# Kernel optimization log

Measured on AMD Instinct MI355X. Metric: run time of the kernel, lower is better.

The kernel has to match this reference:

```python
import jax, jax.numpy as jnp
import numpy as np
import math

B, S, D = 1, 4096, 2048
H, KVH, HD = 32, 8, 64
W = 512            # sliding window size (== block size)
THETA = 10000.0
EPS = 1e-5
INTER = 5632
PRE_SCALE = 1.0 / math.sqrt(2.0)


def setup_inputs() -> dict:
    key = jax.random.key(0)
    ks = jax.random.split(key, 8)
    def w(k, shape, fan_in):
        return jax.random.normal(k, shape, jnp.float32) * (fan_in ** -0.5)
    return {
        "hidden_states": jax.random.normal(ks[0], (B, S, D), jnp.float32),
        "mixer_norm_w": jnp.ones((D,), jnp.float32),
        "wq": w(ks[1], (D, H * HD), D),
        "wk": w(ks[2], (D, KVH * HD), D),
        "wv": w(ks[3], (D, KVH * HD), D),
        "wo": w(ks[4], (H * HD, D), H * HD),
        "mlp_norm_w": jnp.ones((D,), jnp.float32),
        "w_gate": w(ks[5], (D, 2 * INTER), D),
        "w_down": w(ks[6], (INTER, D), INTER),
    }


def rmsnorm(x, w, eps=EPS):
    return x * jax.lax.rsqrt(jnp.mean(x * x, axis=-1, keepdims=True) + eps) * w


def rope(x):
    # x: [B, S, h, HD]; rotate-half RoPE
    half = HD // 2
    inv_freq = 1.0 / (THETA ** (jnp.arange(0, HD, 2, dtype=jnp.float32) / HD))
    freqs = jnp.arange(S, dtype=jnp.float32)[:, None] * inv_freq[None, :]  # [S, half]
    cos = jnp.cos(freqs)[None, :, None, :]
    sin = jnp.sin(freqs)[None, :, None, :]
    x1, x2 = x[..., :half], x[..., half:]
    return jnp.concatenate([x1 * cos - x2 * sin, x2 * cos + x1 * sin], axis=-1)


def sliding_attention(x, wq, wk, wv, wo):
    # x already pre-scaled; returns attn output (pre /pre_scale)
    q = (x @ wq).reshape(B, S, H, HD)
    k = (x @ wk).reshape(B, S, KVH, HD)
    v = (x @ wv).reshape(B, S, KVH, HD)
    q, k = rope(q), rope(k)
    rep = H // KVH
    k = jnp.repeat(k, rep, axis=2)  # [B,S,H,HD]
    v = jnp.repeat(v, rep, axis=2)
    nb = S // W
    qb = q.reshape(B, nb, W, H, HD)
    kb = k.reshape(B, nb, W, H, HD)
    vb = v.reshape(B, nb, W, H, HD)
    zeros = jnp.zeros((B, 1, W, H, HD), q.dtype)
    kw = jnp.concatenate([jnp.concatenate([zeros, kb[:, :-1]], axis=1), kb], axis=2)  # [B,nb,2W,H,HD]
    vw = jnp.concatenate([jnp.concatenate([zeros, vb[:, :-1]], axis=1), vb], axis=2)
    # local mask [nb, W, 2W]
    blk = jnp.arange(nb)[:, None, None]
    q_pos = blk * W + jnp.arange(W)[None, :, None]
    k_pos = blk * W - W + jnp.arange(2 * W)[None, None, :]
    mask = (k_pos >= 0) & (k_pos <= q_pos) & (q_pos - k_pos < W)
    scores = jnp.einsum("bnqhd,bnkhd->bhnqk", qb, kw) * (HD ** -0.5)
    scores = jnp.where(mask[None, None], scores, jnp.finfo(scores.dtype).min)
    p = jax.nn.softmax(scores, axis=-1)
    out = jnp.einsum("bhnqk,bnkhd->bnqhd", p, vw).reshape(B, S, H * HD)
    return out @ wo


def reference(hidden_states, mixer_norm_w, wq, wk, wv, wo, mlp_norm_w, w_gate, w_down):
    residual = hidden_states
    x = rmsnorm(hidden_states, mixer_norm_w)
    attn_out = sliding_attention(x * PRE_SCALE, wq, wk, wv, wo) / PRE_SCALE
    h = residual + attn_out
    xn = rmsnorm(h, mlp_norm_w)
    gv = xn @ w_gate
    gate, y = gv[..., :INTER], gv[..., INTER:]
    mlp_out = (jax.nn.silu(gate) * y) @ w_down
    return h + mlp_out
```

## Files before the change

### kernel.cpp

```cpp
#include <hip/hip_runtime.h>
#include <stdint.h>

typedef __attribute__((ext_vector_type(8))) short s16x8;
typedef __attribute__((ext_vector_type(4))) float f32x4;

#define GLD_LDS16(gp, lp) __builtin_amdgcn_global_load_lds( \
    (__attribute__((address_space(1))) void*)(void*)(gp), \
    (__attribute__((address_space(3))) void*)(lp), 16, 0, 0)

__device__ __forceinline__ float b2f(unsigned short s) {
    unsigned int u = ((unsigned int)s) << 16;
    return __builtin_bit_cast(float, u);
}
__device__ __forceinline__ unsigned short f2b(float f) {
    unsigned int u = __builtin_bit_cast(unsigned int, f);
    u = (u + 0x7FFFu + ((u >> 16) & 1u)) >> 16;
    return (unsigned short)u;
}
__device__ __forceinline__ f32x4 mfma16(s16x8 a, s16x8 b, f32x4 c) {
    return __builtin_amdgcn_mfma_f32_16x16x32_bf16(a, b, c, 0, 0, 0);
}
template <int N> __device__ __forceinline__ void waitvm() {
    if constexpr (N == 2) asm volatile("s_waitcnt vmcnt(2)" ::: "memory");
    else if constexpr (N == 3) asm volatile("s_waitcnt vmcnt(3)" ::: "memory");
    else if constexpr (N == 4) asm volatile("s_waitcnt vmcnt(4)" ::: "memory");
}

__global__ __launch_bounds__(256) void rmsnorm_bf16(
    const float* __restrict__ x, const float* __restrict__ wgt,
    unsigned short* __restrict__ out)
{
    const int row = blockIdx.x;
    const int t = threadIdx.x;
    const float* xr = x + (size_t)row * 2048;
    float4 a = *(const float4*)(xr + t * 8);
    float4 b = *(const float4*)(xr + t * 8 + 4);
    float ss = a.x*a.x + a.y*a.y + a.z*a.z + a.w*a.w
             + b.x*b.x + b.y*b.y + b.z*b.z + b.w*b.w;
    #pragma unroll
    for (int d = 1; d < 64; d <<= 1) ss += __shfl_xor(ss, d);
    __shared__ float red[4];
    if ((t & 63) == 0) red[t >> 6] = ss;
    __syncthreads();
    float tot = red[0] + red[1] + red[2] + red[3];
    float inv = rsqrtf(tot * (1.0f / 2048.0f) + 1e-5f);
    float vals[8] = {a.x, a.y, a.z, a.w, b.x, b.y, b.z, b.w};
    const float* wr_ = wgt + t * 8;
    s16x8 ov;
    #pragma unroll
    for (int j = 0; j < 8; ++j) ov[j] = (short)f2b(vals[j] * inv * wr_[j]);
    *(s16x8*)(out + (size_t)row * 2048 + t * 8) = ov;
}

__global__ __launch_bounds__(256) void transpose_to_bf16(
    const float* __restrict__ in, unsigned short* __restrict__ out, int K, int N)
{
    __shared__ float tile[32][33];
    int n0 = blockIdx.x * 32, k0 = blockIdx.y * 32;
    int r = threadIdx.x >> 5, c = threadIdx.x & 31;
    #pragma unroll
    for (int i = 0; i < 4; ++i)
        tile[r + i * 8][c] = in[(size_t)(k0 + r + i * 8) * N + n0 + c];
    __syncthreads();
    #pragma unroll
    for (int i = 0; i < 4; ++i)
        out[(size_t)(n0 + r + i * 8) * K + k0 + c] = f2b(tile[c][r + i * 8]);
}

template <int BN, int EPI>
__global__ __launch_bounds__(512, 2) void gemmq(
    const unsigned short* __restrict__ A,
    const unsigned short* __restrict__ B,
    void* __restrict__ Cv,
    const float* __restrict__ ADD,
    int N, int K)
{
    constexpr int WN  = BN / 4;
    constexpr int HN  = WN / 2;
    constexpr int NJQ = WN / 32;
    constexpr int LBH = NJQ;
    constexpr int NBU = BN / 64;
    constexpr int ABUF = 256 * 64;
    constexpr int BBUF = BN * 64;
    __shared__ __align__(16) unsigned short As[2 * ABUF];
    __shared__ __align__(16) unsigned short Bs[2 * BBUF];

    const int t = threadIdx.x;
    const int l = t & 63, w = t >> 6;
    const int l15 = l & 15, lg = l >> 4;
    const int wr = w >> 2, wc = w & 3;
    const int x7 = l15 & 7;
    const int cc0 = ((lg) ^ x7) << 3;
    const int cc1 = ((4 | lg) ^ x7) << 3;

    const int nwg = (int)gridDim.x;
    const int orig = (int)blockIdx.x;
    const int q8 = nwg >> 3, r8 = nwg & 7;
    const int xcd = orig & 7, lid = orig >> 3;
    const int wg = (xcd < r8 ? xcd * (q8 + 1) : r8 * (q8 + 1) + (xcd - r8) * q8) + lid;
    const int m0 = (wg & 15) * 256;
    const int n0 = (wg >> 4) * BN;

    const int tr = t >> 3;
    const int scol = ((t & 7) ^ (tr & 7)) << 3;
    const unsigned short* pA[4];
    #pragma unroll
    for (int u = 0; u < 4; ++u) {
        const int lrow = u * 64 + tr;
        const int g = ((lrow >> 6) & 1) * 128 + (lrow >> 7) * 64 + (lrow & 63);
        pA[u] = A + (size_t)(m0 + g) * K + scol;
    }
    const unsigned short* pB[NBU];
    #pragma unroll
    for (int u = 0; u < NBU; ++u) {
        const int lrow = u * 64 + tr;
        const int h = lrow / (BN / 2), rem = lrow % (BN / 2);
        const int g = (rem / HN) * WN + h * HN + (rem % HN);
        pB[u] = B + (size_t)(n0 + g) * K + scol;
    }

    f32x4 acc[2][2][4][NJQ] = {};
    s16x8 aF[4][2];
    s16x8 bF[2][NJQ][2];

    const int NT = K / 64;

    GLD_LDS16(pA[0], &As[0 * 4096 + t * 8]);
    GLD_LDS16(pA[1], &As[1 * 4096 + t * 8]);
    #pragma unroll
    for (int u = 0; u < NBU / 2; ++u) GLD_LDS16(pB[u], &Bs[u * 4096 + t * 8]);
    GLD_LDS16(pA[2], &As[2 * 4096 + t * 8]);
    GLD_LDS16(pA[3], &As[3 * 4096 + t * 8]);
    #pragma unroll
    for (int u = NBU / 2; u < NBU; ++u) GLD_LDS16(pB[u], &Bs[u * 4096 + t * 8]);
    waitvm<2 + LBH>();
    __builtin_amdgcn_s_barrier();

    for (int kt = 0; kt < NT; ++kt) {
        const int rb  = (kt & 1) ? ABUF : 0;
        const int rbB = (kt & 1) ? BBUF : 0;
        const int wb  = ABUF - rb;
        const int wbB = BBUF - rbB;
        const int knext = (kt + 1 < NT ? kt + 1 : kt) * 64;

        #pragma unroll
        for (int i = 0; i < 4; ++i) {
            const int lr = wr * 64 + i * 16 + l15;
            aF[i][0] = *(const s16x8*)&As[rb + lr * 64 + cc0];
            aF[i][1] = *(const s16x8*)&As[rb + lr * 64 + cc1];
        }
        #pragma unroll
        for (int j = 0; j < NJQ; ++j) {
            const int lr = wc * HN + j * 16 + l15;
            bF[0][j][0] = *(const s16x8*)&Bs[rbB + lr * 64 + cc0];
            bF[0][j][1] = *(const s16x8*)&Bs[rbB + lr * 64 + cc1];
        }
        GLD_LDS16(pA[0] + knext, &As[wb + 0 * 4096 + t * 8]);
        GLD_LDS16(pA[1] + knext, &As[wb + 1 * 4096 + t * 8]);
        if constexpr (NJQ == 2) asm volatile("s_waitcnt lgkmcnt(8)" ::: "memory");
        __builtin_amdgcn_s_barrier();
        asm volatile("s_waitcnt lgkmcnt(0)" ::: "memory");
        __builtin_amdgcn_sched_barrier(0);
        __builtin_amdgcn_s_setprio(1);
        #pragma unroll
        for (int kk = 0; kk < 2; ++kk)
            #pragma unroll
            for (int i = 0; i < 4; ++i)
                #pragma unroll
                for (int j = 0; j < NJQ; ++j)
                    acc[0][0][i][j] = mfma16(aF[i][kk], bF[0][j][kk], acc[0][0][i][j]);
        __builtin_amdgcn_s_setprio(0);
        __builtin_amdgcn_sched_barrier(0);
        waitvm<2>();
        __builtin_amdgcn_s_barrier();

        #pragma unroll
        for (int j = 0; j < NJQ; ++j) {
            const int lr = (BN / 2) + wc * HN + j * 16 + l15;
            bF[1][j][0] = *(const s16x8*)&Bs[rbB + lr * 64 + cc0];
            bF[1][j][1] = *(const s16x8*)&Bs[rbB + lr * 64 + cc1];
        }
        #pragma unroll
        for (int u = 0; u < NBU / 2; ++u)
            GLD_LDS16(pB[u] + knext, &Bs[wbB + u * 4096 + t * 8]);
        __builtin_amdgcn_s_barrier();
        asm volatile("s_waitcnt lgkmcnt(0)" ::: "memory");
        __builtin_amdgcn_sched_barrier(0);
        __builtin_amdgcn_s_setprio(1);
        #pragma unroll
        for (int kk = 0; kk < 2; ++kk)
            #pragma unroll
            for (int i = 0; i < 4; ++i)
                #pragma unroll
                for (int j = 0; j < NJQ; ++j)
                    acc[0][1][i][j] = mfma16(aF[i][kk], bF[1][j][kk], acc[0][1][i][j]);
        __builtin_amdgcn_s_setprio(0);
        __builtin_amdgcn_sched_barrier(0);
        __builtin_amdgcn_s_barrier();

        #pragma unroll
        for (int i = 0; i < 4; ++i) {
            const int lr = 128 + wr * 64 + i * 16 + l15;
            aF[i][0] = *(const s16x8*)&As[rb + lr * 64 + cc0];
            aF[i][1] = *(const s16x8*)&As[rb + lr * 64 + cc1];
        }
        GLD_LDS16(pA[2] + knext, &As[wb + 2 * 4096 + t * 8]);
        GLD_LDS16(pA[3] + knext, &As[wb + 3 * 4096 + t * 8]);
        __builtin_amdgcn_s_barrier();
        asm volatile("s_waitcnt lgkmcnt(0)" ::: "memory");
        __builtin_amdgcn_sched_barrier(0);
        __builtin_amdgcn_s_setprio(1);
        #pragma unroll
        for (int kk = 0; kk < 2; ++kk)
            #pragma unroll
            for (int i = 0; i < 4; ++i)
                #pragma unroll
                for (int j = 0; j < NJQ; ++j)
                    acc[1][0][i][j] = mfma16(aF[i][kk], bF[0][j][kk], acc[1][0][i][j]);
        __builtin_amdgcn_s_setprio(0);
        __builtin_amdgcn_sched_barrier(0);
        __builtin_amdgcn_s_barrier();

        #pragma unroll
        for (int u = NBU / 2; u < NBU; ++u)
            GLD_LDS16(pB[u] + knext, &Bs[wbB + u * 4096 + t * 8]);
        __builtin_amdgcn_s_barrier();
        __builtin_amdgcn_s_setprio(1);
        #pragma unroll
        for (int kk = 0; kk < 2; ++kk)
            #pragma unroll
            for (int i = 0; i < 4; ++i)
                #pragma unroll
                for (int j = 0; j < NJQ; ++j)
                    acc[1][1][i][j] = mfma16(aF[i][kk], bF[1][j][kk], acc[1][1][i][j]);
        __builtin_amdgcn_s_setprio(0);
        __builtin_amdgcn_sched_barrier(0);
        waitvm<2 + LBH>();
        __builtin_amdgcn_s_barrier();
    }

    #pragma unroll
    for (int qm = 0; qm < 2; ++qm)
        #pragma unroll
        for (int i = 0; i < 4; ++i)
            #pragma unroll
            for (int r = 0; r < 4; ++r) {
                const int row = m0 + wr * 128 + qm * 64 + i * 16 + lg * 4 + r;
                const size_t rbase = (size_t)row * N;
                #pragma unroll
                for (int qn = 0; qn < 2; ++qn)
                    #pragma unroll
                    for (int j = 0; j < NJQ; ++j) {
                        const int col = n0 + wc * WN + qn * HN + j * 16 + l15;
                        float v = acc[qm][qn][i][j][r];
                        if constexpr (EPI == 0) {
                            ((unsigned short*)Cv)[rbase + col] = f2b(v);
                        } else if constexpr (EPI == 1) {
                            ((float*)Cv)[rbase + col] = v + ADD[rbase + col];
                        } else {
                            unsigned short* Cb = (unsigned short*)Cv;
                            float y = b2f(Cb[rbase + col]);
                            float sg = v / (1.0f + expf(-v));
                            Cb[rbase + col] = f2b(sg * y);
                        }
                    }
            }
}

__global__ void rope_tab_k(float2* __restrict__ tab) {
    int i = blockIdx.x * 256 + threadIdx.x;
    if (i >= 4096 * 32) return;
    int s = i >> 5, d = i & 31;
    float inv = exp2f(-(float)d * (13.287712379549449f / 32.0f));
    float fr = (float)s * inv;
    float sv, cv;
    sincosf(fr, &sv, &cv);
    tab[i] = make_float2(cv, sv);
}

__global__ void rope_apply_k(unsigned short* __restrict__ qkv, const float2* __restrict__ tab) {
    int i = blockIdx.x * 256 + threadIdx.x;
    if (i >= 4096 * 40 * 4) return;
    int dg = i & 3;
    int rest = i >> 2;
    int head = rest % 40;
    int s = rest / 40;
    int off = head < 32 ? head * 64 : 2048 + (head - 32) * 64;
    unsigned short* p = qkv + (size_t)s * 3072 + off + dg * 8;
    s16x8 x1 = *(const s16x8*)p;
    s16x8 x2 = *(const s16x8*)(p + 32);
    const float2* tb = tab + s * 32 + dg * 8;
    s16x8 o1, o2;
    #pragma unroll
    for (int j = 0; j < 8; ++j) {
        float2 cs = tb[j];
        float a = b2f((unsigned short)x1[j]);
        float b = b2f((unsigned short)x2[j]);
        o1[j] = (short)f2b(a * cs.x - b * cs.y);
        o2[j] = (short)f2b(b * cs.x + a * cs.y);
    }
    *(s16x8*)p = o1;
    *(s16x8*)(p + 32) = o2;
}

__global__ __launch_bounds__(256) void attn_swa(
    const unsigned short* __restrict__ qkv,
    unsigned short* __restrict__ out)
{
    constexpr int LDQ = 3072;
    const int qb = blockIdx.x;
    const int h = blockIdx.y;
    const int kvh = h >> 2;
    const int q0 = qb * 64;
    const int t = threadIdx.x, l = t & 63, w = t >> 6;
    const int l15 = l & 15, lg = l >> 4;

    __shared__ unsigned short Kl[64 * 64];
    __shared__ unsigned short Vt[64 * 72];
    __shared__ unsigned short Pl[4 * 16 * 72];

    s16x8 qf[2];
    {
        const unsigned short* qp = qkv + (size_t)(q0 + w * 16 + l15) * LDQ + h * 64 + lg * 8;
        qf[0] = *(const s16x8*)(qp);
        qf[1] = *(const s16x8*)(qp + 32);
    }
    float m_run[4] = {-1e30f, -1e30f, -1e30f, -1e30f};
    float l_run[4] = {0.f, 0.f, 0.f, 0.f};
    f32x4 o[4] = {};

    const float SC = 0.0625f * 1.4426950408889634f;
    const int kt_lo = qb >= 8 ? qb - 8 : 0;

    for (int kt = kt_lo; kt <= qb; ++kt) {
        const int ks = kt * 64;
        __syncthreads();
        {
            const unsigned short* kg = qkv + (size_t)(ks + (t >> 3)) * LDQ + 2048 + kvh * 64 + (t & 7) * 8;
            GLD_LDS16(kg, Kl + t * 8);
            GLD_LDS16(kg + (size_t)32 * LDQ, Kl + t * 8 + 2048);
        }
        {
            const unsigned short* vg = qkv + (size_t)(ks + l) * LDQ + 2560 + kvh * 64 + w * 16;
            s16x8 v0 = *(const s16x8*)vg;
            s16x8 v1 = *(const s16x8*)(vg + 8);
            #pragma unroll
            for (int j = 0; j < 8; ++j) Vt[(w * 16 + j) * 72 + l] = (unsigned short)v0[j];
            #pragma unroll
            for (int j = 0; j < 8; ++j) Vt[(w * 16 + 8 + j) * 72 + l] = (unsigned short)v1[j];
        }
        __syncthreads();

        f32x4 sf[4] = {};
        #pragma unroll
        for (int kf = 0; kf < 4; ++kf) {
            #pragma unroll
            for (int kk = 0; kk < 2; ++kk) {
                s16x8 kb = *(const s16x8*)(Kl + (kf * 16 + l15) * 64 + kk * 32 + lg * 8);
                sf[kf] = mfma16(qf[kk], kb, sf[kf]);
            }
        }

        float tmax[4];
        #pragma unroll
        for (int r = 0; r < 4; ++r) {
            int qrow = q0 + w * 16 + lg * 4 + r;
            float mx = -1e30f;
            #pragma unroll
            for (int kf = 0; kf < 4; ++kf) {
                int key = ks + kf * 16 + l15;
                bool valid = (key <= qrow) && (qrow - key < 512);
                if (valid) mx = fmaxf(mx, sf[kf][r]);
            }
            #pragma unroll
            for (int d2 = 1; d2 < 16; d2 <<= 1) mx = fmaxf(mx, __shfl_xor(mx, d2));
            tmax[r] = mx;
        }

        float alpha[4], rsum[4];
        #pragma unroll
        for (int r = 0; r < 4; ++r) {
            float mnew = fmaxf(m_run[r], tmax[r]);
            alpha[r] = exp2f((m_run[r] - mnew) * SC);
            m_run[r] = mnew;
            rsum[r] = 0.f;
        }

        unsigned short* Pw = Pl + w * (16 * 72);
        #pragma unroll
        for (int kf = 0; kf < 4; ++kf) {
            #pragma unroll
            for (int r = 0; r < 4; ++r) {
                int qrow = q0 + w * 16 + lg * 4 + r;
                int key = ks + kf * 16 + l15;
                bool valid = (key <= qrow) && (qrow - key < 512);
                float p = valid ? exp2f((sf[kf][r] - m_run[r]) * SC) : 0.f;
                rsum[r] += p;
                Pw[(lg * 4 + r) * 72 + kf * 16 + l15] = f2b(p);
            }
        }
        #pragma unroll
        for (int r = 0; r < 4; ++r) {
            #pragma unroll
            for (int d2 = 1; d2 < 16; d2 <<= 1) rsum[r] += __shfl_xor(rsum[r], d2);
            l_run[r] = l_run[r] * alpha[r] + rsum[r];
        }
        #pragma unroll
        for (int hf = 0; hf < 4; ++hf)
            #pragma unroll
            for (int r = 0; r < 4; ++r) o[hf][r] *= alpha[r];

        asm volatile("s_waitcnt lgkmcnt(0)" ::: "memory");
        __builtin_amdgcn_sched_barrier(0);

        #pragma unroll
        for (int kk2 = 0; kk2 < 2; ++kk2) {
            s16x8 pa = *(const s16x8*)(Pw + l15 * 72 + kk2 * 32 + lg * 8);
            #pragma unroll
            for (int hf = 0; hf < 4; ++hf) {
                s16x8 vb = *(const s16x8*)(Vt + (hf * 16 + l15) * 72 + kk2 * 32 + lg * 8);
                o[hf] = mfma16(pa, vb, o[hf]);
            }
        }
    }

    #pragma unroll
    for (int r = 0; r < 4; ++r) {
        int qrow = q0 + w * 16 + lg * 4 + r;
        float invl = 1.0f / l_run[r];
        unsigned short* orow = out + (size_t)qrow * 2048 + h * 64;
        #pragma unroll
        for (int hf = 0; hf < 4; ++hf)
            orow[hf * 16 + l15] = f2b(o[hf][r] * invl);
    }
}

extern "C" void kernel_launch(void* const* d_in, const int* in_sizes, int n_in,
                              void* d_out, int out_size, void* d_ws, size_t ws_size,
                              hipStream_t stream)
{
    const float* hidden = (const float*)d_in[0];
    const float* w_mix  = (const float*)d_in[1];
    const float* wq     = (const float*)d_in[2];
    const float* wk     = (const float*)d_in[3];
    const float* wv     = (const float*)d_in[4];
    const float* wo     = (const float*)d_in[5];
    const float* w_mlp  = (const float*)d_in[6];
    const float* wg     = (const float*)d_in[7];
    const float* wd     = (const float*)d_in[8];
    float* out = (float*)d_out;

    char* ws = (char*)d_ws;
    size_t off = 0;
    auto alloc = [&](size_t bytes) {
        char* p = ws + off;
        off += (bytes + 255) & ~(size_t)255;
        return p;
    };
    unsigned short* Wt   = (unsigned short*)alloc((size_t)11264 * 2048 * 2);
    unsigned short* xn   = (unsigned short*)alloc((size_t)4096 * 2048 * 2);
    unsigned short* qkv  = (unsigned short*)alloc((size_t)4096 * 3072 * 2);
    float2*         rtab = (float2*)alloc((size_t)4096 * 32 * 8);
    unsigned short* attn = (unsigned short*)alloc((size_t)4096 * 2048 * 2);
    float*          hbuf = (float*)alloc((size_t)4096 * 2048 * 4);
    unsigned short* act  = (unsigned short*)alloc((size_t)4096 * 5632 * 2);

    rmsnorm_bf16<<<4096, 256, 0, stream>>>(hidden, w_mix, xn);

    transpose_to_bf16<<<dim3(64, 64), 256, 0, stream>>>(wq, Wt, 2048, 2048);
    transpose_to_bf16<<<dim3(16, 64), 256, 0, stream>>>(wk, Wt + (size_t)2048 * 2048, 2048, 512);
    transpose_to_bf16<<<dim3(16, 64), 256, 0, stream>>>(wv, Wt + (size_t)2560 * 2048, 2048, 512);

    gemmq<256, 0><<<192, 512, 0, stream>>>(xn, Wt, qkv, nullptr, 3072, 2048);

    rope_tab_k<<<(4096 * 32 + 255) / 256, 256, 0, stream>>>(rtab);
    rope_apply_k<<<(4096 * 40 * 4 + 255) / 256, 256, 0, stream>>>(qkv, rtab);

    attn_swa<<<dim3(64, 32), 256, 0, stream>>>(qkv, attn);

    transpose_to_bf16<<<dim3(64, 64), 256, 0, stream>>>(wo, Wt, 2048, 2048);
    gemmq<128, 1><<<256, 512, 0, stream>>>(attn, Wt, hbuf, hidden, 2048, 2048);

    rmsnorm_bf16<<<4096, 256, 0, stream>>>(hbuf, w_mlp, xn);

    transpose_to_bf16<<<dim3(352, 64), 256, 0, stream>>>(wg, Wt, 2048, 11264);
    gemmq<256, 0><<<352, 512, 0, stream>>>(xn, Wt + (size_t)5632 * 2048, act, nullptr, 5632, 2048);
    gemmq<256, 2><<<352, 512, 0, stream>>>(xn, Wt, act, nullptr, 5632, 2048);

    transpose_to_bf16<<<dim3(64, 176), 256, 0, stream>>>(wd, Wt, 5632, 2048);
    gemmq<128, 1><<<256, 512, 0, stream>>>(act, Wt, out, hbuf, 2048, 5632);
}
```

Measured before the change: 637.9 us.

## Fuse gate and up GEMMs into one GLU kernel and restructure gemmq pipeline waits

Adds a gemm_glu kernel that computes the gate and up projections together in one pass, sharing the A tile, and applies SiLU(gate)*y in the epilogue. This replaces two GEMM launches and the bf16 round-trip of the y half through global memory. The gemmq main loop is also reorganised: all B sub-tiles are now loaded in a single phase, the explicit lgkmcnt waits and sched_barriers are removed, and vmcnt thresholds are tuned per BN. The risks are that dropping the LDS waits leaves the ordering to the compiler, and that the doubled accumulators in gemm_glu raise register pressure.

After: 551.8 us. 1.16x faster.

```diff
diff --git a/kernel.cpp b/kernel.cpp
--- a/kernel.cpp
+++ b/kernel.cpp
@@ -21,9 +21,9 @@
     return __builtin_amdgcn_mfma_f32_16x16x32_bf16(a, b, c, 0, 0, 0);
 }
 template <int N> __device__ __forceinline__ void waitvm() {
-    if constexpr (N == 2) asm volatile("s_waitcnt vmcnt(2)" ::: "memory");
-    else if constexpr (N == 3) asm volatile("s_waitcnt vmcnt(3)" ::: "memory");
+    if constexpr (N == 3) asm volatile("s_waitcnt vmcnt(3)" ::: "memory");
     else if constexpr (N == 4) asm volatile("s_waitcnt vmcnt(4)" ::: "memory");
+    else if constexpr (N == 6) asm volatile("s_waitcnt vmcnt(6)" ::: "memory");
 }
 
 __global__ __launch_bounds__(256) void rmsnorm_bf16(
@@ -78,10 +78,12 @@
     constexpr int WN  = BN / 4;
     constexpr int HN  = WN / 2;
     constexpr int NJQ = WN / 32;
-    constexpr int LBH = NJQ;
     constexpr int NBU = BN / 64;
     constexpr int ABUF = 256 * 64;
     constexpr int BBUF = BN * 64;
+    constexpr int W_P0 = 4;
+    constexpr int W_P1 = (BN == 256) ? 6 : 4;
+    constexpr int W_P2 = (BN == 256) ? 4 : 3;
     __shared__ __align__(16) unsigned short As[2 * ABUF];
     __shared__ __align__(16) unsigned short Bs[2 * BBUF];
 
@@ -128,12 +130,10 @@
     GLD_LDS16(pA[0], &As[0 * 4096 + t * 8]);
     GLD_LDS16(pA[1], &As[1 * 4096 + t * 8]);
     #pragma unroll
-    for (int u = 0; u < NBU / 2; ++u) GLD_LDS16(pB[u], &Bs[u * 4096 + t * 8]);
+    for (int u = 0; u < NBU; ++u) GLD_LDS16(pB[u], &Bs[u * 4096 + t * 8]);
     GLD_LDS16(pA[2], &As[2 * 4096 + t * 8]);
     GLD_LDS16(pA[3], &As[3 * 4096 + t * 8]);
-    #pragma unroll
-    for (int u = NBU / 2; u < NBU; ++u) GLD_LDS16(pB[u], &Bs[u * 4096 + t * 8]);
-    waitvm<2 + LBH>();
+    waitvm<W_P2>();
     __builtin_amdgcn_s_barrier();
 
     for (int kt = 0; kt < NT; ++kt) {
@@ -157,10 +157,7 @@
         }
         GLD_LDS16(pA[0] + knext, &As[wb + 0 * 4096 + t * 8]);
         GLD_LDS16(pA[1] + knext, &As[wb + 1 * 4096 + t * 8]);
-        if constexpr (NJQ == 2) asm volatile("s_waitcnt lgkmcnt(8)" ::: "memory");
-        __builtin_amdgcn_s_barrier();
-        asm volatile("s_waitcnt lgkmcnt(0)" ::: "memory");
-        __builtin_amdgcn_sched_barrier(0);
+        __builtin_amdgcn_s_barrier();
         __builtin_amdgcn_s_setprio(1);
         #pragma unroll
         for (int kk = 0; kk < 2; ++kk)
@@ -170,8 +167,7 @@
                 for (int j = 0; j < NJQ; ++j)
                     acc[0][0][i][j] = mfma16(aF[i][kk], bF[0][j][kk], acc[0][0][i][j]);
         __builtin_amdgcn_s_setprio(0);
-        __builtin_amdgcn_sched_barrier(0);
-        waitvm<2>();
+        waitvm<W_P0>();
         __builtin_amdgcn_s_barrier();
 
         #pragma unroll
@@ -181,11 +177,9 @@
             bF[1][j][1] = *(const s16x8*)&Bs[rbB + lr * 64 + cc1];
         }
         #pragma unroll
-        for (int u = 0; u < NBU / 2; ++u)
+        for (int u = 0; u < NBU; ++u)
             GLD_LDS16(pB[u] + knext, &Bs[wbB + u * 4096 + t * 8]);
         __builtin_amdgcn_s_barrier();
-        asm volatile("s_waitcnt lgkmcnt(0)" ::: "memory");
-        __builtin_amdgcn_sched_barrier(0);
         __builtin_amdgcn_s_setprio(1);
         #pragma unroll
         for (int kk = 0; kk < 2; ++kk)
@@ -195,7 +189,7 @@
                 for (int j = 0; j < NJQ; ++j)
                     acc[0][1][i][j] = mfma16(aF[i][kk], bF[1][j][kk], acc[0][1][i][j]);
         __builtin_amdgcn_s_setprio(0);
-        __builtin_amdgcn_sched_barrier(0);
+        waitvm<W_P1>();
         __builtin_amdgcn_s_barrier();
 
         #pragma unroll
@@ -207,8 +201,6 @@
         GLD_LDS16(pA[2] + knext, &As[wb + 2 * 4096 + t * 8]);
         GLD_LDS16(pA[3] + knext, &As[wb + 3 * 4096 + t * 8]);
         __builtin_amdgcn_s_barrier();
-        asm volatile("s_waitcnt lgkmcnt(0)" ::: "memory");
-        __builtin_amdgcn_sched_barrier(0);
         __builtin_amdgcn_s_setprio(1);
         #pragma unroll
         for (int kk = 0; kk < 2; ++kk)
@@ -217,15 +209,6 @@
                 #pragma unroll
                 for (int j = 0; j < NJQ; ++j)
                     acc[1][0][i][j] = mfma16(aF[i][kk], bF[0][j][kk], acc[1][0][i][j]);
-        __builtin_amdgcn_s_setprio(0);
-        __builtin_amdgcn_sched_barrier(0);
-        __builtin_amdgcn_s_barrier();
-
-        #pragma unroll
-        for (int u = NBU / 2; u < NBU; ++u)
-            GLD_LDS16(pB[u] + knext, &Bs[wbB + u * 4096 + t * 8]);
-        __builtin_amdgcn_s_barrier();
-        __builtin_amdgcn_s_setprio(1);
         #pragma unroll
         for (int kk = 0; kk < 2; ++kk)
             #pragma unroll
@@ -234,8 +217,7 @@
                 for (int j = 0; j < NJQ; ++j)
                     acc[1][1][i][j] = mfma16(aF[i][kk], bF[1][j][kk], acc[1][1][i][j]);
         __builtin_amdgcn_s_setprio(0);
-        __builtin_amdgcn_sched_barrier(0);
-        waitvm<2 + LBH>();
+        waitvm<W_P2>();
         __builtin_amdgcn_s_barrier();
     }
 
@@ -255,15 +237,180 @@
                         float v = acc[qm][qn][i][j][r];
                         if constexpr (EPI == 0) {
                             ((unsigned short*)Cv)[rbase + col] = f2b(v);
-                        } else if constexpr (EPI == 1) {
+                        } else {
                             ((float*)Cv)[rbase + col] = v + ADD[rbase + col];
-                        } else {
-                            unsigned short* Cb = (unsigned short*)Cv;
-                            float y = b2f(Cb[rbase + col]);
-                            float sg = v / (1.0f + expf(-v));
-                            Cb[rbase + col] = f2b(sg * y);
                         }
                     }
+            }
+}
+
+__global__ __launch_bounds__(512, 2) void gemm_glu(
+    const unsigned short* __restrict__ A,
+    const unsigned short* __restrict__ Bg,
+    const unsigned short* __restrict__ By,
+    unsigned short* __restrict__ act,
+    int N, int K)
+{
+    constexpr int ABUF = 256 * 64, BBUF = 128 * 64;
+    __shared__ __align__(16) unsigned short As[2 * ABUF];
+    __shared__ __align__(16) unsigned short Bgs[2 * BBUF];
+    __shared__ __align__(16) unsigned short Bys[2 * BBUF];
+
+    const int t = threadIdx.x;
+    const int l = t & 63, w = t >> 6;
+    const int l15 = l & 15, lg = l >> 4;
+    const int wr = w >> 2, wc = w & 3;
+    const int x7 = l15 & 7;
+    const int cc0 = ((lg) ^ x7) << 3;
+    const int cc1 = ((4 | lg) ^ x7) << 3;
+
+    const int nwg = (int)gridDim.x;
+    const int orig = (int)blockIdx.x;
+    const int q8 = nwg >> 3;
+    const int xcd = orig & 7, lid = orig >> 3;
+    const int wg = xcd * q8 + lid;
+    const int m0 = (wg & 15) * 256;
+    const int n0 = (wg >> 4) * 128;
+
+    const int tr = t >> 3;
+    const int scol = ((t & 7) ^ (tr & 7)) << 3;
+    const unsigned short* pA[4];
+    #pragma unroll
+    for (int u = 0; u < 4; ++u) {
+        const int lrow = u * 64 + tr;
+        const int g = ((lrow >> 6) & 1) * 128 + (lrow >> 7) * 64 + (lrow & 63);
+        pA[u] = A + (size_t)(m0 + g) * K + scol;
+    }
+    const unsigned short *pG[2], *pY[2];
+    #pragma unroll
+    for (int u = 0; u < 2; ++u) {
+        const int g = (tr >> 4) * 32 + u * 16 + (tr & 15);
+        pG[u] = Bg + (size_t)(n0 + g) * K + scol;
+        pY[u] = By + (size_t)(n0 + g) * K + scol;
+    }
+
+    f32x4 accG[2][2][4] = {};
+    f32x4 accY[2][2][4] = {};
+    s16x8 aF[4][2];
+    s16x8 gF[2][2], yF[2][2];
+
+    const int NT = K / 64;
+
+    GLD_LDS16(pA[0], &As[0 * 4096 + t * 8]);
+    GLD_LDS16(pA[1], &As[1 * 4096 + t * 8]);
+    GLD_LDS16(pG[0], &Bgs[0 * 4096 + t * 8]);
+    GLD_LDS16(pY[0], &Bys[0 * 4096 + t * 8]);
+    GLD_LDS16(pG[1], &Bgs[1 * 4096 + t * 8]);
+    GLD_LDS16(pY[1], &Bys[1 * 4096 + t * 8]);
+    GLD_LDS16(pA[2], &As[2 * 4096 + t * 8]);
+    GLD_LDS16(pA[3], &As[3 * 4096 + t * 8]);
+    waitvm<4>();
+    __builtin_amdgcn_s_barrier();
+
+    for (int kt = 0; kt < NT; ++kt) {
+        const int rb  = (kt & 1) ? ABUF : 0;
+        const int rbB = (kt & 1) ? BBUF : 0;
+        const int wb  = ABUF - rb;
+        const int wbB = BBUF - rbB;
+        const int knext = (kt + 1 < NT ? kt + 1 : kt) * 64;
+
+        #pragma unroll
+        for (int i = 0; i < 4; ++i) {
+            const int lr = wr * 64 + i * 16 + l15;
+            aF[i][0] = *(const s16x8*)&As[rb + lr * 64 + cc0];
+            aF[i][1] = *(const s16x8*)&As[rb + lr * 64 + cc1];
+        }
+        {
+            const int lr = wc * 16 + l15;
+            gF[0][0] = *(const s16x8*)&Bgs[rbB + lr * 64 + cc0];
+            gF[0][1] = *(const s16x8*)&Bgs[rbB + lr * 64 + cc1];
+            yF[0][0] = *(const s16x8*)&Bys[rbB + lr * 64 + cc0];
+            yF[0][1] = *(const s16x8*)&Bys[rbB + lr * 64 + cc1];
+        }
+        GLD_LDS16(pA[0] + knext, &As[wb + 0 * 4096 + t * 8]);
+        GLD_LDS16(pA[1] + knext, &As[wb + 1 * 4096 + t * 8]);
+        __builtin_amdgcn_s_barrier();
+        __builtin_amdgcn_s_setprio(1);
+        #pragma unroll
+        for (int kk = 0; kk < 2; ++kk)
+            #pragma unroll
+            for (int i = 0; i < 4; ++i) {
+                accG[0][0][i] = mfma16(aF[i][kk], gF[0][kk], accG[0][0][i]);
+                accY[0][0][i] = mfma16(aF[i][kk], yF[0][kk], accY[0][0][i]);
+            }
+        __builtin_amdgcn_s_setprio(0);
+        waitvm<4>();
+        __builtin_amdgcn_s_barrier();
+
+        {
+            const int lr = 64 + wc * 16 + l15;
+            gF[1][0] = *(const s16x8*)&Bgs[rbB + lr * 64 + cc0];
+            gF[1][1] = *(const s16x8*)&Bgs[rbB + lr * 64 + cc1];
+            yF[1][0] = *(const s16x8*)&Bys[rbB + lr * 64 + cc0];
+            yF[1][1] = *(const s16x8*)&Bys[rbB + lr * 64 + cc1];
+        }
+        GLD_LDS16(pG[0] + knext, &Bgs[wbB + 0 * 4096 + t * 8]);
+        GLD_LDS16(pY[0] + knext, &Bys[wbB + 0 * 4096 + t * 8]);
+        GLD_LDS16(pG[1] + knext, &Bgs[wbB + 1 * 4096 + t * 8]);
+        GLD_LDS16(pY[1] + knext, &Bys[wbB + 1 * 4096 + t * 8]);
+        __builtin_amdgcn_s_barrier();
+        __builtin_amdgcn_s_setprio(1);
+        #pragma unroll
+        for (int kk = 0; kk < 2; ++kk)
+            #pragma unroll
+            for (int i = 0; i < 4; ++i) {
+                accG[0][1][i] = mfma16(aF[i][kk], gF[1][kk], accG[0][1][i]);
+                accY[0][1][i] = mfma16(aF[i][kk], yF[1][kk], accY[0][1][i]);
+            }
+        __builtin_amdgcn_s_setprio(0);
+        waitvm<6>();
+        __builtin_amdgcn_s_barrier();
+
+        #pragma unroll
+        for (int i = 0; i < 4; ++i) {
+            const int lr = 128 + wr * 64 + i * 16 + l15;
+            aF[i][0] = *(const s16x8*)&As[rb + lr * 64 + cc0];
+            aF[i][1] = *(const s16x8*)&As[rb + lr * 64 + cc1];
+        }
+        GLD_LDS16(pA[2] + knext, &As[wb + 2 * 4096 + t * 8]);
+        GLD_LDS16(pA[3] + knext, &As[wb + 3 * 4096 + t * 8]);
+        __builtin_amdgcn_s_barrier();
+        __builtin_amdgcn_s_setprio(1);
+        #pragma unroll
+        for (int kk = 0; kk < 2; ++kk)
+            #pragma unroll
+            for (int i = 0; i < 4; ++i) {
+                accG[1][0][i] = mfma16(aF[i][kk], gF[0][kk], accG[1][0][i]);
+                accY[1][0][i] = mfma16(aF[i][kk], yF[0][kk], accY[1][0][i]);
+            }
+        #pragma unroll
+        for (int kk = 0; kk < 2; ++kk)
+            #pragma unroll
+            for (int i = 0; i < 4; ++i) {
+                accG[1][1][i] = mfma16(aF[i][kk], gF[1][kk], accG[1][1][i]);
+                accY[1][1][i] = mfma16(aF[i][kk], yF[1][kk], accY[1][1][i]);
+            }
+        __builtin_amdgcn_s_setprio(0);
+        waitvm<4>();
+        __builtin_amdgcn_s_barrier();
+    }
+
+    #pragma unroll
+    for (int qm = 0; qm < 2; ++qm)
+        #pragma unroll
+        for (int i = 0; i < 4; ++i)
+            #pragma unroll
+            for (int r = 0; r < 4; ++r) {
+                const int row = m0 + wr * 128 + qm * 64 + i * 16 + lg * 4 + r;
+                const size_t rbase = (size_t)row * N;
+                #pragma unroll
+                for (int qn = 0; qn < 2; ++qn) {
+                    const int col = n0 + wc * 32 + qn * 16 + l15;
+                    float g = accG[qm][qn][i][r];
+                    float y = accY[qm][qn][i][r];
+                    float sg = g / (1.0f + expf(-g));
+                    act[rbase + col] = f2b(sg * y);
+                }
             }
 }
 
@@ -484,8 +631,7 @@
     rmsnorm_bf16<<<4096, 256, 0, stream>>>(hbuf, w_mlp, xn);
 
     transpose_to_bf16<<<dim3(352, 64), 256, 0, stream>>>(wg, Wt, 2048, 11264);
-    gemmq<256, 0><<<352, 512, 0, stream>>>(xn, Wt + (size_t)5632 * 2048, act, nullptr, 5632, 2048);
-    gemmq<256, 2><<<352, 512, 0, stream>>>(xn, Wt, act, nullptr, 5632, 2048);
+    gemm_glu<<<704, 512, 0, stream>>>(xn, Wt, Wt + (size_t)5632 * 2048, act, 5632, 2048);
 
     transpose_to_bf16<<<dim3(64, 176), 256, 0, stream>>>(wd, Wt, 5632, 2048);
     gemmq<128, 1><<<256, 512, 0, stream>>>(act, Wt, out, hbuf, 2048, 5632);
```
